# Kernel optimization log

Measured on AMD Instinct MI355X. Metric: run time of the kernel, lower is better.

The kernel has to match this reference:

```python
import jax, jax.numpy as jnp
import numpy as np

NUM_VOCAB = 50000
EMBED_DIM = 128
SENT_SIZE = 50
MAX_HOPS = 3
BATCH = 128
MEM_SIZE = 200


def position_encoding(sentence_size, embedding_dim):
    # vectorized version of the original double loop
    i = np.arange(1, embedding_dim + 1, dtype=np.float32)[:, None]  # [D,1]
    j = np.arange(1, sentence_size + 1, dtype=np.float32)[None, :]  # [1,S]
    enc = (i - (embedding_dim + 1) / 2.0) * (j - (sentence_size + 1) / 2.0)
    enc = 1.0 + 4.0 * enc / embedding_dim / sentence_size
    enc[:, -1] = 1.0
    return np.transpose(enc).astype(np.float32)  # [S,D]


def setup_inputs() -> dict:
    key = jax.random.key(0)
    k1, k2, k3, k4, k5 = jax.random.split(key, 5)
    story = jax.random.randint(k1, (BATCH, MEM_SIZE, SENT_SIZE), 0, NUM_VOCAB, dtype=jnp.int64)
    query = jax.random.randint(k2, (BATCH, SENT_SIZE), 0, NUM_VOCAB, dtype=jnp.int64)
    # max_hops+1 embedding tables, N(0, 0.1), padding_idx=0 row zeroed
    C = 0.1 * jax.random.normal(k3, (MAX_HOPS + 1, NUM_VOCAB, EMBED_DIM), dtype=jnp.float32)
    C = C.at[:, 0, :].set(0.0)
    # T_k linear layer (PyTorch default uniform init bound)
    bound = 1.0 / np.sqrt(EMBED_DIM)
    T_w = jax.random.uniform(k4, (EMBED_DIM, EMBED_DIM), jnp.float32, -bound, bound)
    T_b = jax.random.uniform(k5, (EMBED_DIM,), jnp.float32, -bound, bound)
    return {"story": story, "query": query, "C": C, "T_w": T_w, "T_b": T_b}


def reference(story, query, C, T_w, T_b):
    enc = jnp.asarray(position_encoding(SENT_SIZE, EMBED_DIM))  # [S,D]
    # u0: position-encoded sum of query embedding
    q_emb = C[0][query]  # [B,S,D]
    u = jnp.einsum('bsd,sd->bd', q_emb, enc)
    for hop in range(MAX_HOPS):
        emb_A = C[hop][story]          # [B,M,S,D]
        m_A = jnp.einsum('bmsd,sd->bmd', emb_A, enc)
        prob = jax.nn.softmax(jnp.einsum('bmd,bd->bm', m_A, u), axis=-1)
        emb_C = C[hop + 1][story]      # [B,M,S,D]
        m_C = jnp.einsum('bmsd,sd->bmd', emb_C, enc)
        o_k = jnp.einsum('bmd,bm->bd', m_C, prob)
        t_k = jax.nn.sigmoid(u @ T_w.T + T_b)
        u = (1.0 - t_k) * u + o_k * t_k
    a_hat = u @ C[MAX_HOPS].T  # [B,V]
    return a_hat
```

## Files before the change

### kernel.cpp

```cpp
#include <hip/hip_runtime.h>
#include <cstdint>
#include <cstddef>

#define NV 50000
#define ED 128
#define SS 50
#define NB 128
#define NM 200
#define BMD (NB*NM*ED)
#define NCH 32
#define CHD 1563

__global__ __launch_bounds__(256) void story_embed_k(
    const int* __restrict__ story, const float* __restrict__ C,
    float* __restrict__ Mt) {
  const int wave = threadIdx.x >> 6;
  const int lane = threadIdx.x & 63;
  const int bm0 = blockIdx.x * 16;
  const int sl = (lane < SS) ? lane : (SS - 1);

  int idxg[4], cidg[4];
#pragma unroll
  for (int gg = 0; gg < 4; ++gg) {
    const int bm = bm0 + wave + 4 * gg;
    idxg[gg] = story[(size_t)bm * SS + sl];
    cidg[gg] = (lane < SS) ? (idxg[gg] / CHD) : -1;
  }
  const float a0 = ((float)(2*lane + 1) - 64.5f) * 6.25e-4f;
  const float a1 = ((float)(2*lane + 2) - 64.5f) * 6.25e-4f;
  float2 acc[4][4];
#pragma unroll
  for (int gg = 0; gg < 4; ++gg)
#pragma unroll
    for (int k = 0; k < 4; ++k) acc[gg][k] = make_float2(0.f, 0.f);

  for (int c = 0; c < NCH; ++c) {
#pragma unroll
    for (int gg = 0; gg < 4; ++gg) {
      unsigned long long mask = __ballot(cidg[gg] == c);
      while (mask) {
        const int s = __builtin_ctzll(mask);
        mask &= mask - 1;
        const int row = __shfl(idxg[gg], s);
        float e0, e1;
        if (s == SS - 1) { e0 = 1.0f; e1 = 1.0f; }
        else {
          float js = (float)(s + 1) - 25.5f;
          e0 = fmaf(a0, js, 1.0f);
          e1 = fmaf(a1, js, 1.0f);
        }
        const float* base = C + (size_t)row * ED + 2 * lane;
#pragma unroll
        for (int k = 0; k < 4; ++k) {
          float2 cv = *(const float2*)(base + (size_t)k * NV * ED);
          acc[gg][k].x = fmaf(e0, cv.x, acc[gg][k].x);
          acc[gg][k].y = fmaf(e1, cv.y, acc[gg][k].y);
        }
      }
    }
    __syncthreads();
  }

#pragma unroll
  for (int gg = 0; gg < 4; ++gg) {
    const int bm = bm0 + wave + 4 * gg;
#pragma unroll
    for (int k = 0; k < 4; ++k)
      *(float2*)(Mt + (size_t)k * BMD + (size_t)bm * ED + 2 * lane) = acc[gg][k];
  }
}

__global__ __launch_bounds__(512, 2) void hops_k(
    const int* __restrict__ query, const float* __restrict__ C,
    const float* __restrict__ Tw, const float* __restrict__ Tb,
    const float* __restrict__ Mt, float* __restrict__ U) {
  const int b = blockIdx.x;
  const int tid = threadIdx.x;
  const int d = tid & 127;
  const int p = tid >> 7;
  const int wave = tid >> 6, lane = tid & 63;
  __shared__ float tile[NM * ED];
  __shared__ float u[ED];
  __shared__ float part[512];
  __shared__ float sc[NM];
  __shared__ float o[ED];

  {
    const float4* s4 = (const float4*)(Mt + (size_t)b * NM * ED);
    float4* t4 = (float4*)tile;
    float4 st[13];
#pragma unroll
    for (int j = 0; j < 13; ++j) {
      int i = tid + 512 * j;
      st[j] = (i < NM * ED / 4) ? s4[i] : make_float4(0.f, 0.f, 0.f, 0.f);
    }
#pragma unroll
    for (int j = 0; j < 13; ++j) {
      int i = tid + 512 * j;
      if (i < NM * ED / 4) t4[i] = st[j];
    }
  }

  {
    const float ad = ((float)(d + 1) - 64.5f) * 6.25e-4f;
    int rows[13];
#pragma unroll
    for (int j = 0; j < 13; ++j) {
      int s = p + 4 * j;
      rows[j] = query[b * SS + (s < SS ? s : 0)];
    }
    float cv[13];
#pragma unroll
    for (int j = 0; j < 13; ++j)
      cv[j] = C[(size_t)rows[j] * ED + d];
    float accv = 0.f;
#pragma unroll
    for (int j = 0; j < 13; ++j) {
      int s = p + 4 * j;
      float e;
      if (s >= SS) e = 0.f;
      else if (s == SS - 1) e = 1.0f;
      else e = fmaf(ad, (float)(s + 1) - 25.5f, 1.0f);
      accv = fmaf(e, cv[j], accv);
    }
    part[tid] = accv;
  }
  __syncthreads();
  if (tid < ED)
    u[tid] = part[tid] + part[tid + 128] + part[tid + 256] + part[tid + 384];
  __syncthreads();

  for (int hop = 0; hop < 3; ++hop) {
    const float* Tn = Mt + (size_t)(hop + 1) * BMD + (size_t)b * NM * ED;
    float pf[50];
#pragma unroll
    for (int j = 0; j < 50; ++j)
      pf[j] = Tn[(size_t)(p + 4 * j) * ED + d];

    {
      float u0v = u[2 * lane], u1v = u[2 * lane + 1];
      for (int m = wave; m < NM; m += 16) {
        const int m2 = m + 8;
        const bool has2 = (m2 < NM);
        float2 r0 = *(const float2*)&tile[m * ED + 2 * lane];
        float pa = r0.x * u0v + r0.y * u1v;
        float pb = 0.f;
        if (has2) {
          float2 r1 = *(const float2*)&tile[m2 * ED + 2 * lane];
          pb = r1.x * u0v + r1.y * u1v;
        }
#pragma unroll
        for (int off = 32; off; off >>= 1) {
          pa += __shfl_xor(pa, off);
          pb += __shfl_xor(pb, off);
        }
        if (lane == 0) {
          sc[m] = pa;
          if (has2) sc[m2] = pb;
        }
      }
    }
    __syncthreads();

    float v = (tid < NM) ? sc[tid] : -1e30f;
    {
      float t = v;
#pragma unroll
      for (int off = 32; off; off >>= 1) t = fmaxf(t, __shfl_xor(t, off));
      if (lane == 0) part[wave] = t;
    }
    __syncthreads();
    float mx = part[0];
#pragma unroll
    for (int w = 1; w < 8; ++w) mx = fmaxf(mx, part[w]);
    float ev = 0.f;
    if (tid < NM) { ev = __expf(v - mx); sc[tid] = ev; }
    {
      float t = ev;
#pragma unroll
      for (int off = 32; off; off >>= 1) t += __shfl_xor(t, off);
      if (lane == 0) part[8 + wave] = t;
    }
    __syncthreads();
    float tot = part[8];
#pragma unroll
    for (int w = 9; w < 16; ++w) tot += part[w];
    const float inv = 1.0f / tot;
    __syncthreads();

    {
      float oacc = 0.f;
#pragma unroll
      for (int j = 0; j < 50; ++j)
        oacc = fmaf(sc[p + 4 * j], pf[j], oacc);
      part[tid] = oacc;
    }
    if (hop < 2) {
#pragma unroll
      for (int j = 0; j < 50; ++j)
        tile[(p + 4 * j) * ED + d] = pf[j];
    }
    __syncthreads();
    if (tid < ED)
      o[tid] = (part[tid] + part[tid + 128] + part[tid + 256] + part[tid + 384])
               * inv;
    __syncthreads();

    {
      const float4* twr = (const float4*)(Tw + (size_t)d * ED + p * 32);
      float4 tw4[8];
#pragma unroll
      for (int j = 0; j < 8; ++j) tw4[j] = twr[j];
      float tacc = 0.f;
#pragma unroll
      for (int j = 0; j < 8; ++j) {
        tacc = fmaf(u[p * 32 + 4 * j + 0], tw4[j].x, tacc);
        tacc = fmaf(u[p * 32 + 4 * j + 1], tw4[j].y, tacc);
        tacc = fmaf(u[p * 32 + 4 * j + 2], tw4[j].z, tacc);
        tacc = fmaf(u[p * 32 + 4 * j + 3], tw4[j].w, tacc);
      }
      part[tid] = tacc;
    }
    __syncthreads();
    if (tid < ED) {
      float dot = part[tid] + part[tid + 128] + part[tid + 256] + part[tid + 384]
                  + Tb[tid];
      float tk = 1.0f / (1.0f + __expf(-dot));
      u[tid] = (1.0f - tk) * u[tid] + o[tid] * tk;
    }
    __syncthreads();
  }
  if (tid < ED) U[(size_t)b * ED + tid] = u[tid];
}

#define OSTR 132
__global__ __launch_bounds__(256) void out_mm_k(
    const float* __restrict__ U, const float* __restrict__ C3,
    float* __restrict__ out) {
  __shared__ float ut[ED * OSTR];
  __shared__ float ct[ED * OSTR];
  const int tid = threadIdx.x;
  const int v0 = blockIdx.x * 128;
  const int vcnt = min(128, NV - v0);

#pragma unroll
  for (int bt = 0; bt < 4; ++bt) {
    float tmp[16];
#pragma unroll
    for (int j = 0; j < 16; ++j)
      tmp[j] = U[tid + 256 * (bt * 16 + j)];
#pragma unroll
    for (int j = 0; j < 16; ++j) {
      int i = tid + 256 * (bt * 16 + j);
      ut[(i & 127) * OSTR + (i >> 7)] = tmp[j];
    }
  }
#pragma unroll
  for (int bt = 0; bt < 4; ++bt) {
    float tmp[16];
#pragma unroll
    for (int j = 0; j < 16; ++j) {
      int i = tid + 256 * (bt * 16 + j);
      tmp[j] = (i < vcnt * ED) ? C3[(size_t)v0 * ED + i] : 0.f;
    }
#pragma unroll
    for (int j = 0; j < 16; ++j) {
      int i = tid + 256 * (bt * 16 + j);
      ct[(i & 127) * OSTR + (i >> 7)] = tmp[j];
    }
  }
  __syncthreads();

  const int vb = (tid & 15) * 8;
  const int bb = (tid >> 4) * 8;
  float acc[8][8];
#pragma unroll
  for (int i = 0; i < 8; ++i)
#pragma unroll
    for (int j = 0; j < 8; ++j) acc[i][j] = 0.f;

  for (int dd = 0; dd < ED; ++dd) {
    float4 c0 = *(const float4*)&ct[dd * OSTR + vb];
    float4 c1 = *(const float4*)&ct[dd * OSTR + vb + 4];
    float4 u0 = *(const float4*)&ut[dd * OSTR + bb];
    float4 u1 = *(const float4*)&ut[dd * OSTR + bb + 4];
    float cv[8] = {c0.x, c0.y, c0.z, c0.w, c1.x, c1.y, c1.z, c1.w};
    float uv[8] = {u0.x, u0.y, u0.z, u0.w, u1.x, u1.y, u1.z, u1.w};
#pragma unroll
    for (int i = 0; i < 8; ++i)
#pragma unroll
      for (int j = 0; j < 8; ++j) acc[i][j] = fmaf(uv[i], cv[j], acc[i][j]);
  }

  if (vcnt == 128) {
#pragma unroll
    for (int i = 0; i < 8; ++i) {
      float4 r0 = make_float4(acc[i][0], acc[i][1], acc[i][2], acc[i][3]);
      float4 r1 = make_float4(acc[i][4], acc[i][5], acc[i][6], acc[i][7]);
      float* op = &out[(size_t)(bb + i) * NV + v0 + vb];
      *(float4*)op = r0;
      *(float4*)(op + 4) = r1;
    }
  } else {
#pragma unroll
    for (int i = 0; i < 8; ++i)
      for (int j = 0; j < 8; ++j)
        if (v0 + vb + j < NV)
          out[(size_t)(bb + i) * NV + v0 + vb + j] = acc[i][j];
  }
}

extern "C" void kernel_launch(void* const* d_in, const int* in_sizes, int n_in,
                              void* d_out, int out_size, void* d_ws, size_t ws_size,
                              hipStream_t stream) {
  const int*   story = (const int*)d_in[0];
  const int*   query = (const int*)d_in[1];
  const float* C     = (const float*)d_in[2];
  const float* Tw    = (const float*)d_in[3];
  const float* Tb    = (const float*)d_in[4];
  float* out = (float*)d_out;

  float* wsf = (float*)d_ws;
  float* Mt  = wsf;
  float* U   = wsf + (size_t)4 * BMD;

  hipLaunchKernelGGL(story_embed_k, dim3(NB * NM / 16), dim3(256), 0, stream,
                     story, C, Mt);
  hipLaunchKernelGGL(hops_k, dim3(NB), dim3(512), 0, stream,
                     query, C, Tw, Tb, Mt, U);
  hipLaunchKernelGGL(out_mm_k, dim3((NV + 127) / 128), dim3(256), 0, stream,
                     U, C + (size_t)3 * NV * ED, out);
}
```

Before: 440.0 us.

## Use fp16 MFMA for output projection with pre-converted C3 table

Replaces the scalar FP32 register-tiled output GEMM (u @ C3^T) with an MFMA 16x16x32 f16 kernel. A new kernel converts the C3 embedding table to fp16 into workspace each call, and U is converted to fp16 in shared memory. The goal is to move the GEMM onto matrix cores and halve C3 read traffic inside the GEMM. In exchange it adds a full conversion pass over C3 and lowers input precision to fp16, which may affect accuracy. The output stores are per-column scalar writes strided by NV.

```diff
diff --git a/kernel.cpp b/kernel.cpp
--- a/kernel.cpp
+++ b/kernel.cpp
@@ -10,6 +10,10 @@
 #define BMD (NB*NM*ED)
 #define NCH 32
 #define CHD 1563
+
+typedef _Float16 f16x8 __attribute__((ext_vector_type(8)));
+typedef _Float16 f16x4 __attribute__((ext_vector_type(4)));
+typedef float    f32x4 __attribute__((ext_vector_type(4)));
 
 __global__ __launch_bounds__(256) void story_embed_k(
     const int* __restrict__ story, const float* __restrict__ C,
@@ -233,80 +237,69 @@
   if (tid < ED) U[(size_t)b * ED + tid] = u[tid];
 }
 
-#define OSTR 132
-__global__ __launch_bounds__(256) void out_mm_k(
-    const float* __restrict__ U, const float* __restrict__ C3,
+__global__ __launch_bounds__(256) void cvt_c3_k(
+    const float* __restrict__ src, _Float16* __restrict__ dst) {
+  const int i = blockIdx.x * 256 + threadIdx.x;
+  const float4* s4 = (const float4*)src;
+  float4 f0 = s4[2 * i];
+  float4 f1 = s4[2 * i + 1];
+  f16x8 h;
+  h[0] = (_Float16)f0.x; h[1] = (_Float16)f0.y;
+  h[2] = (_Float16)f0.z; h[3] = (_Float16)f0.w;
+  h[4] = (_Float16)f1.x; h[5] = (_Float16)f1.y;
+  h[6] = (_Float16)f1.z; h[7] = (_Float16)f1.w;
+  *(f16x8*)(dst + (size_t)8 * i) = h;
+}
+
+__global__ __launch_bounds__(256) void out_mm_mfma_k(
+    const float* __restrict__ U, const _Float16* __restrict__ C3h,
     float* __restrict__ out) {
-  __shared__ float ut[ED * OSTR];
-  __shared__ float ct[ED * OSTR];
+  __shared__ _Float16 Ub[ED * 136];
   const int tid = threadIdx.x;
-  const int v0 = blockIdx.x * 128;
-  const int vcnt = min(128, NV - v0);
-
-#pragma unroll
-  for (int bt = 0; bt < 4; ++bt) {
-    float tmp[16];
-#pragma unroll
-    for (int j = 0; j < 16; ++j)
-      tmp[j] = U[tid + 256 * (bt * 16 + j)];
+
+  {
+    const float4* u4 = (const float4*)U;
 #pragma unroll
     for (int j = 0; j < 16; ++j) {
-      int i = tid + 256 * (bt * 16 + j);
-      ut[(i & 127) * OSTR + (i >> 7)] = tmp[j];
-    }
-  }
-#pragma unroll
-  for (int bt = 0; bt < 4; ++bt) {
-    float tmp[16];
-#pragma unroll
-    for (int j = 0; j < 16; ++j) {
-      int i = tid + 256 * (bt * 16 + j);
-      tmp[j] = (i < vcnt * ED) ? C3[(size_t)v0 * ED + i] : 0.f;
-    }
-#pragma unroll
-    for (int j = 0; j < 16; ++j) {
-      int i = tid + 256 * (bt * 16 + j);
-      ct[(i & 127) * OSTR + (i >> 7)] = tmp[j];
+      int i = tid + 256 * j;
+      float4 f = u4[i];
+      int row = i >> 5;
+      int col = (i & 31) * 4;
+      f16x4 h;
+      h[0] = (_Float16)f.x; h[1] = (_Float16)f.y;
+      h[2] = (_Float16)f.z; h[3] = (_Float16)f.w;
+      *(f16x4*)&Ub[row * 136 + col] = h;
     }
   }
   __syncthreads();
 
-  const int vb = (tid & 15) * 8;
-  const int bb = (tid >> 4) * 8;
-  float acc[8][8];
-#pragma unroll
-  for (int i = 0; i < 8; ++i)
-#pragma unroll
-    for (int j = 0; j < 8; ++j) acc[i][j] = 0.f;
-
-  for (int dd = 0; dd < ED; ++dd) {
-    float4 c0 = *(const float4*)&ct[dd * OSTR + vb];
-    float4 c1 = *(const float4*)&ct[dd * OSTR + vb + 4];
-    float4 u0 = *(const float4*)&ut[dd * OSTR + bb];
-    float4 u1 = *(const float4*)&ut[dd * OSTR + bb + 4];
-    float cv[8] = {c0.x, c0.y, c0.z, c0.w, c1.x, c1.y, c1.z, c1.w};
-    float uv[8] = {u0.x, u0.y, u0.z, u0.w, u1.x, u1.y, u1.z, u1.w};
-#pragma unroll
-    for (int i = 0; i < 8; ++i)
-#pragma unroll
-      for (int j = 0; j < 8; ++j) acc[i][j] = fmaf(uv[i], cv[j], acc[i][j]);
-  }
-
-  if (vcnt == 128) {
-#pragma unroll
-    for (int i = 0; i < 8; ++i) {
-      float4 r0 = make_float4(acc[i][0], acc[i][1], acc[i][2], acc[i][3]);
-      float4 r1 = make_float4(acc[i][4], acc[i][5], acc[i][6], acc[i][7]);
-      float* op = &out[(size_t)(bb + i) * NV + v0 + vb];
-      *(float4*)op = r0;
-      *(float4*)(op + 4) = r1;
-    }
-  } else {
-#pragma unroll
-    for (int i = 0; i < 8; ++i)
-      for (int j = 0; j < 8; ++j)
-        if (v0 + vb + j < NV)
-          out[(size_t)(bb + i) * NV + v0 + vb + j] = acc[i][j];
+  const int wave = tid >> 6, lane = tid & 63;
+  const int n = lane & 15, q = lane >> 4;
+  const int v = blockIdx.x * 64 + wave * 16 + n;
+  const bool vok = (v < NV);
+
+  f32x4 acc[8];
+#pragma unroll
+  for (int mt = 0; mt < 8; ++mt) acc[mt] = (f32x4){0.f, 0.f, 0.f, 0.f};
+
+#pragma unroll
+  for (int kt = 0; kt < 4; ++kt) {
+    f16x8 bfrag = {};
+    if (vok) bfrag = *(const f16x8*)(C3h + (size_t)v * ED + kt * 32 + q * 8);
+#pragma unroll
+    for (int mt = 0; mt < 8; ++mt) {
+      f16x8 afrag = *(const f16x8*)&Ub[(mt * 16 + n) * 136 + kt * 32 + q * 8];
+      acc[mt] = __builtin_amdgcn_mfma_f32_16x16x32_f16(afrag, bfrag, acc[mt],
+                                                       0, 0, 0);
+    }
+  }
+
+  if (vok) {
+#pragma unroll
+    for (int mt = 0; mt < 8; ++mt)
+#pragma unroll
+      for (int i = 0; i < 4; ++i)
+        out[(size_t)(mt * 16 + q * 4 + i) * NV + v] = acc[mt][i];
   }
 }
 
@@ -321,13 +314,16 @@
   float* out = (float*)d_out;
 
   float* wsf = (float*)d_ws;
-  float* Mt  = wsf;
-  float* U   = wsf + (size_t)4 * BMD;
+  float*     Mt  = wsf;
+  float*     U   = wsf + (size_t)4 * BMD;
+  _Float16*  C3h = (_Float16*)(wsf + (size_t)4 * BMD + NB * ED);
 
   hipLaunchKernelGGL(story_embed_k, dim3(NB * NM / 16), dim3(256), 0, stream,
                      story, C, Mt);
   hipLaunchKernelGGL(hops_k, dim3(NB), dim3(512), 0, stream,
                      query, C, Tw, Tb, Mt, U);
-  hipLaunchKernelGGL(out_mm_k, dim3((NV + 127) / 128), dim3(256), 0, stream,
-                     U, C + (size_t)3 * NV * ED, out);
-}
+  hipLaunchKernelGGL(cvt_c3_k, dim3(NV * ED / 8 / 256), dim3(256), 0, stream,
+                     C + (size_t)3 * NV * ED, C3h);
+  hipLaunchKernelGGL(out_mm_mfma_k, dim3((NV + 63) / 64), dim3(256), 0, stream,
+                     U, C3h, out);
+}
```

Result: faster. 409.8 us (-6.9%).
